# Kernel tuning notes

Measured on AMD Instinct MI355X. Metric: run time of the kernel, lower is better.

## Reference

```python
import jax, jax.numpy as jnp
import numpy as np

H, C, D, F = 8, 1024, 128, 512  # num_heads, num_chanels, out_dim, featurs_dim
B = 16


def setup_inputs() -> dict:
    key = jax.random.key(0)
    ks = jax.random.split(key, 9)
    s = 0.02
    return {
        "x": jax.random.normal(ks[0], (B, C, F), jnp.float32),
        "Wk": jax.random.normal(ks[1], (F, H * D), jnp.float32) * s,
        "bk": jax.random.normal(ks[2], (H * D,), jnp.float32) * s,
        "Wq": jax.random.normal(ks[3], (F, H * D), jnp.float32) * s,
        "bq": jax.random.normal(ks[4], (H * D,), jnp.float32) * s,
        "Wv": jax.random.normal(ks[5], (F, H * D), jnp.float32) * s,
        "bv": jax.random.normal(ks[6], (H * D,), jnp.float32) * s,
        "Ww0": jax.random.normal(ks[7], (H * D, D), jnp.float32) * s,
        "bw0": jax.random.normal(ks[8], (D,), jnp.float32) * s,
    }


def reference(x, Wk, bk, Wq, bq, Wv, bv, Ww0, bw0):
    # Linear projections on last dim: [B, C, H*D]
    # NOTE: the original reshapes [B, C, H*D] -> [B, H, C, D] WITHOUT a permute,
    # which mixes channel/head axes; we replicate that exactly.
    k = (x @ Wk + bk).reshape(-1, H, C, D)
    q = (x @ Wq + bq).reshape(-1, H, C, D)
    v = (x @ Wv + bv).reshape(-1, H, C, D)
    scores = jnp.einsum('bhcf,bhdf->bhcd', q, k) / jnp.sqrt(jnp.float32(D))
    att = jax.nn.softmax(scores, axis=-1) - jnp.eye(C, dtype=scores.dtype)
    vals = jnp.einsum('bhcd,bhdf->bhcf', att, v)          # [B, H, C, D]
    vals = vals.transpose(0, 2, 1, 3).reshape(vals.shape[0], C, H * D)
    return vals @ Ww0 + bw0                                # [B, C, D]
```

## Files before the change

kernel.cpp:

```cpp
#include <hip/hip_runtime.h>
#include <hip/hip_bf16.h>
#include <cstdint>
#include <cstddef>

using u16 = unsigned short;
typedef __attribute__((ext_vector_type(4))) float f32x4;
typedef __attribute__((ext_vector_type(16))) float f32x16;
typedef __attribute__((ext_vector_type(8))) unsigned short u16x8;
typedef __attribute__((ext_vector_type(4))) unsigned short u16x4;
typedef __attribute__((ext_vector_type(4))) unsigned int u32x4;
typedef __bf16 bfrag __attribute__((ext_vector_type(8)));

constexpr int Hn = 8, Cn = 1024, Dn = 128, Fn = 512, Bn = 16;
constexpr int M1 = Bn * Cn;

constexpr size_t OFF_XB  = 0;
constexpr size_t SZ_XB   = (size_t)M1 * Fn * 2;
constexpr size_t OFF_WT  = OFF_XB + SZ_XB;
constexpr size_t SZ_WT   = 3ull * 1024 * 512 * 2;
constexpr size_t OFF_W0T = OFF_WT + SZ_WT;
constexpr size_t SZ_W0T  = 128ull * 1024 * 2;
constexpr size_t OFF_Q   = OFF_W0T + SZ_W0T;
constexpr size_t SZ_P    = (size_t)Bn * Hn * Cn * Dn * 2;
constexpr size_t OFF_K   = OFF_Q + SZ_P;
constexpr size_t OFF_V   = OFF_K + SZ_P;
constexpr size_t OFF_ATT = OFF_V + SZ_P;

__device__ __forceinline__ float bf2f(u16 u) {
  unsigned int x = ((unsigned int)u) << 16;
  return __builtin_bit_cast(float, x);
}
__device__ __forceinline__ u16 f2bf(float f) {
  unsigned int u = __builtin_bit_cast(unsigned int, f);
  u += 0x7fffu + ((u >> 16) & 1u);
  return (u16)(u >> 16);
}
__device__ __forceinline__ f32x4 mfma16(bfrag a, bfrag b, f32x4 c) {
  return __builtin_amdgcn_mfma_f32_16x16x32_bf16(a, b, c, 0, 0, 0);
}
__device__ __forceinline__ f32x16 mfma32(bfrag a, bfrag b, f32x16 c) {
  return __builtin_amdgcn_mfma_f32_32x32x16_bf16(a, b, c, 0, 0, 0);
}
__device__ __forceinline__ void gload16(const void* g, void* lds) {
  __builtin_amdgcn_global_load_lds(
      (const __attribute__((address_space(1))) unsigned int*)g,
      (__attribute__((address_space(3))) unsigned int*)lds, 16, 0, 0);
}
__device__ __forceinline__ unsigned cvtpk(float lo, float hi) {
  unsigned r;
  asm("v_cvt_pk_bf16_f32 %0, %1, %2" : "=v"(r) : "v"(lo), "v"(hi));
  return r;
}

__global__ void cvt_bf16(const float* __restrict__ in, u16* __restrict__ out, int n) {
  int idx = (blockIdx.x * blockDim.x + threadIdx.x) * 4;
  if (idx < n) {
    float4 v = *(const float4*)(in + idx);
    u16x4 o;
    o.x = f2bf(v.x); o.y = f2bf(v.y); o.z = f2bf(v.z); o.w = f2bf(v.w);
    *(u16x4*)(out + idx) = o;
  }
}

__global__ void transpose_cvt(const float* __restrict__ in, u16* __restrict__ out,
                              int R, int Cc) {
  __shared__ float tile[32][33];
  int c0 = blockIdx.x * 32, r0 = blockIdx.y * 32;
  int tx = threadIdx.x, ty = threadIdx.y;
#pragma unroll
  for (int i = 0; i < 4; ++i)
    tile[ty + i * 8][tx] = in[(size_t)(r0 + ty + i * 8) * Cc + c0 + tx];
  __syncthreads();
#pragma unroll
  for (int i = 0; i < 4; ++i)
    out[(size_t)(c0 + ty + i * 8) * R + r0 + tx] = f2bf(tile[tx][ty + i * 8]);
}

__global__ void vtrans(const u16* __restrict__ in, u16* __restrict__ out) {
  __shared__ u16 tile[32][33];
  int d0 = blockIdx.x * 32, c0 = blockIdx.y * 32, bh = blockIdx.z;
  const u16* ip = in + (size_t)bh * (Cn * Dn);
  u16* op = out + (size_t)bh * (Dn * Cn);
  int tx = threadIdx.x, ty = threadIdx.y;
#pragma unroll
  for (int i = 0; i < 4; ++i)
    tile[ty + i * 8][tx] = ip[(size_t)(c0 + ty + i * 8) * Dn + d0 + tx];
  __syncthreads();
#pragma unroll
  for (int i = 0; i < 4; ++i)
    op[(size_t)(d0 + ty + i * 8) * Cn + c0 + tx] = tile[tx][ty + i * 8];
}

__global__ void qkv_gemm(const u16* __restrict__ xb, const u16* __restrict__ wt,
                         const float* __restrict__ bq, const float* __restrict__ bk,
                         const float* __restrict__ bv,
                         u16* __restrict__ qout, u16* __restrict__ kout,
                         u16* __restrict__ vout) {
  __shared__ u16 As[128 * 64];
  __shared__ u16 Bs[128 * 64];
  const int m0 = blockIdx.x * 128;
  const int n0 = blockIdx.y * 128;
  const int p  = blockIdx.z;
  const u16* wp = wt + (size_t)p * 1024 * 512;
  const float* bias = (p == 0) ? bq : (p == 1) ? bk : bv;
  u16* outp = (p == 0) ? qout : (p == 1) ? kout : vout;
  const float osc = (p == 0) ? 0.12751744116389548f : 1.0f;

  const int tid = threadIdx.x, l = tid & 63, w = tid >> 6;
  const int lr = l & 15, lg = l >> 4;
  const int wr = w >> 1, wc = w & 1;

  f32x4 acc[4][4] = {};

  for (int kt = 0; kt < Fn; kt += 64) {
#pragma unroll
    for (int i = 0; i < 4; ++i) {
      int chb = (i * 4 + w) * 64;
      int ch = chb + l;
      int row = ch >> 3, scc = (ch & 7) ^ (row & 7);
      gload16(xb + (size_t)(m0 + row) * Fn + kt + scc * 8, &As[chb * 8]);
    }
#pragma unroll
    for (int i = 0; i < 4; ++i) {
      int chb = (i * 4 + w) * 64;
      int ch = chb + l;
      int row = ch >> 3, scc = (ch & 7) ^ (row & 7);
      gload16(wp + (size_t)(n0 + row) * Fn + kt + scc * 8, &Bs[chb * 8]);
    }
    __syncthreads();
#pragma unroll
    for (int kk = 0; kk < 2; ++kk) {
      bfrag af[4], bf_[4];
#pragma unroll
      for (int fm = 0; fm < 4; ++fm) {
        int row = wr * 64 + fm * 16 + lr;
        int off = (kk * 4 + lg) ^ (row & 7);
        af[fm] = *(const bfrag*)&As[row * 64 + off * 8];
      }
#pragma unroll
      for (int fn = 0; fn < 4; ++fn) {
        int row = wc * 64 + fn * 16 + lr;
        int off = (kk * 4 + lg) ^ (row & 7);
        bf_[fn] = *(const bfrag*)&Bs[row * 64 + off * 8];
      }
#pragma unroll
      for (int fm = 0; fm < 4; ++fm)
#pragma unroll
        for (int fn = 0; fn < 4; ++fn)
          acc[fm][fn] = mfma16(af[fm], bf_[fn], acc[fm][fn]);
    }
    __syncthreads();
  }

#pragma unroll
  for (int fm = 0; fm < 4; ++fm) {
#pragma unroll
    for (int r = 0; r < 4; ++r) {
      int m = m0 + wr * 64 + fm * 16 + lg * 4 + r;
      int b = m >> 10, c = m & 1023;
      int gh = c >> 7;
#pragma unroll
      for (int fn = 0; fn < 4; ++fn) {
        int j = n0 + wc * 64 + fn * 16 + lr;
        float v = (acc[fm][fn][r] + bias[j]) * osc;
        int ii = ((c & 127) << 3) | (j >> 7);
        int d = j & 127;
        size_t idx = (((size_t)(b * 8 + gh) * 1024 + ii) << 7) | d;
        outp[idx] = f2bf(v);
      }
    }
  }
}

__global__ __launch_bounds__(256, 2)
void attn_kernel(const u16* __restrict__ qp_all, const u16* __restrict__ kp_all,
                 const u16* __restrict__ vt_all, u16* __restrict__ attout) {
  __shared__ u16 smem[2 * 16384];

  const int bid = blockIdx.x;
  const int wg = (bid & 7) * 128 + (bid >> 3);
  const int bh = wg >> 3;
  const int qt = wg & 7;

  const int tid = threadIdx.x, l = tid & 63, w = tid >> 6;
  const int q31 = l & 31, hi = l >> 5;

  const u16* qp  = qp_all + (size_t)bh * (Cn * Dn);
  const u16* kp  = kp_all + (size_t)bh * (Cn * Dn);
  const u16* vtp = vt_all + (size_t)bh * (Dn * Cn);
  const int qr0 = qt * 128 + w * 32;

  auto stage = [&](int t2, int b) {
    const u16* kb = kp + (size_t)t2 * 64 * 128;
    const u16* vb = vtp + (size_t)t2 * 64;
    u16* KsD = smem + b * 16384;
    u16* VsD = smem + b * 16384 + 8192;
#pragma unroll
    for (int c = 0; c < 4; ++c) {
      int ch = c * 256 + tid;
      int row = ch >> 4, scc = (ch & 15) ^ (row & 15);
      gload16(kb + row * 128 + scc * 8, KsD + (c * 256 + w * 64) * 8);
    }
#pragma unroll
    for (int c = 0; c < 4; ++c) {
      int ch = c * 256 + tid;
      int row = ch >> 3, scc = (ch & 7) ^ (row & 7);
      gload16(vb + (size_t)row * 1024 + scc * 8, VsD + (c * 256 + w * 64) * 8);
    }
  };

  bfrag aq[8];
#pragma unroll
  for (int kk = 0; kk < 8; ++kk)
    aq[kk] = *(const bfrag*)(qp + (size_t)(qr0 + q31) * Dn + kk * 16 + hi * 8);

  f32x16 ot[4] = {};
  float mst = -1e30f, lst = 0.f;

  stage(0, 0);
  __syncthreads();

  for (int t = 0; t < 16; ++t) {
    const int cur = t & 1;
    const u16* Ks = smem + cur * 16384;
    const u16* Vs = smem + cur * 16384 + 8192;
    if (t < 15) stage(t + 1, cur ^ 1);

    f32x16 st[2] = {};
    __builtin_amdgcn_s_setprio(1);
#pragma unroll
    for (int tt = 0; tt < 2; ++tt) {
#pragma unroll
      for (int kk = 0; kk < 8; ++kk) {
        int row = tt * 32 + q31;
        int off = (2 * kk + hi) ^ (row & 15);
        bfrag kf = *(const bfrag*)&Ks[row * 128 + off * 8];
        st[tt] = mfma32(kf, aq[kk], st[tt]);
      }
    }
    __builtin_amdgcn_s_setprio(0);

    float mx = st[0][0];
#pragma unroll
    for (int r = 1; r < 16; ++r) mx = fmaxf(mx, st[0][r]);
#pragma unroll
    for (int r = 0; r < 16; ++r) mx = fmaxf(mx, st[1][r]);
    mx = fmaxf(mx, __shfl_xor(mx, 32, 64));
    if (!__all(mx <= mst + 8.f)) {
      float mnew = fmaxf(mst, mx);
      float alpha = exp2f(mst - mnew);
      lst *= alpha;
#pragma unroll
      for (int dt = 0; dt < 4; ++dt)
#pragma unroll
        for (int r = 0; r < 16; ++r) ot[dt][r] *= alpha;
      mst = mnew;
    }
    float rs = 0.f;
#pragma unroll
    for (int tt = 0; tt < 2; ++tt)
#pragma unroll
      for (int r = 0; r < 16; ++r) {
        float pv = exp2f(st[tt][r] - mst);
        st[tt][r] = pv;
        rs += pv;
      }
    rs += __shfl_xor(rs, 32, 64);
    lst += rs;

    bfrag pb[4];
#pragma unroll
    for (int tt = 0; tt < 2; ++tt) {
      unsigned c[8];
#pragma unroll
      for (int m = 0; m < 8; ++m)
        c[m] = cvtpk(st[tt][2 * m], st[tt][2 * m + 1]);
#pragma unroll
      for (int kkt = 0; kkt < 2; ++kkt) {
        unsigned a0 = c[4 * kkt + 0], b0 = c[4 * kkt + 2];
        unsigned a1 = c[4 * kkt + 1], b1 = c[4 * kkt + 3];
        asm("v_permlane32_swap_b32 %0, %1" : "+v"(a0), "+v"(b0));
        asm("v_permlane32_swap_b32 %0, %1" : "+v"(a1), "+v"(b1));
        u32x4 bw; bw.x = a0; bw.y = a1; bw.z = b0; bw.w = b1;
        pb[tt * 2 + kkt] = __builtin_bit_cast(bfrag, bw);
      }
    }

    __builtin_amdgcn_s_setprio(1);
#pragma unroll
    for (int kk = 0; kk < 4; ++kk) {
#pragma unroll
      for (int dt = 0; dt < 4; ++dt) {
        int d = dt * 32 + q31;
        int off = (2 * kk + hi) ^ (d & 7);
        bfrag vf = *(const bfrag*)&Vs[d * 64 + off * 8];
        ot[dt] = mfma32(vf, pb[kk], ot[dt]);
      }
    }
    __builtin_amdgcn_s_setprio(0);
    __syncthreads();
  }

  const float linv = 1.f / lst;
  const int c1 = qr0 + q31;
  u16* my = smem + w * 4096;
#pragma unroll
  for (int dt = 0; dt < 4; ++dt)
#pragma unroll
    for (int rp = 0; rp < 8; ++rp) {
      int reg = 2 * rp;
      int d = dt * 32 + (reg & 3) + 8 * (reg >> 2) + 4 * hi;
      float v0 = bf2f(vtp[((size_t)d << 10) | c1]);
      float v1 = bf2f(vtp[((size_t)(d + 1) << 10) | c1]);
      unsigned pk = cvtpk(ot[dt][reg] * linv - v0, ot[dt][reg + 1] * linv - v1);
      *(unsigned*)&my[q31 * 128 + (((d >> 3) ^ (q31 & 7)) << 3) + (d & 7)] = pk;
    }
  const int b = bh >> 3, h = bh & 7;
#pragma unroll
  for (int it = 0; it < 8; ++it) {
    int rowq = it * 4 + (l >> 4);
    int ch = l & 15;
    u16x8 rd = *(const u16x8*)&my[rowq * 128 + ((ch ^ (rowq & 7))) * 8];
    int cg = qr0 + rowq;
    *(u16x8*)&attout[(((size_t)(b * 1024 + cg)) * 8 + h) * 128 + ch * 8] = rd;
  }
}

__global__ void out_gemm(const u16* __restrict__ A, const u16* __restrict__ Bt,
                         const float* __restrict__ bias, float* __restrict__ out) {
  __shared__ u16 As[64 * 64];
  __shared__ u16 Bs[128 * 64];
  const int m0 = blockIdx.x * 64;
  const int tid = threadIdx.x, l = tid & 63, w = tid >> 6;
  const int lr = l & 15, lg = l >> 4;
  const int wr = w >> 1, wc = w & 1;
  f32x4 acc[2][4] = {};

  for (int kt = 0; kt < 1024; kt += 64) {
#pragma unroll
    for (int i = 0; i < 2; ++i) {
      int chb = (i * 4 + w) * 64;
      int ch = chb + l;
      int row = ch >> 3, scc = (ch & 7) ^ (row & 7);
      gload16(A + (size_t)(m0 + row) * 1024 + kt + scc * 8, &As[chb * 8]);
    }
#pragma unroll
    for (int i = 0; i < 4; ++i) {
      int chb = (i * 4 + w) * 64;
      int ch = chb + l;
      int row = ch >> 3, scc = (ch & 7) ^ (row & 7);
      gload16(Bt + (size_t)row * 1024 + kt + scc * 8, &Bs[chb * 8]);
    }
    __syncthreads();
#pragma unroll
    for (int kk = 0; kk < 2; ++kk) {
      bfrag af[2], bf_[4];
#pragma unroll
      for (int fm = 0; fm < 2; ++fm) {
        int row = wr * 32 + fm * 16 + lr;
        int off = (kk * 4 + lg) ^ (row & 7);
        af[fm] = *(const bfrag*)&As[row * 64 + off * 8];
      }
#pragma unroll
      for (int fn = 0; fn < 4; ++fn) {
        int row = wc * 64 + fn * 16 + lr;
        int off = (kk * 4 + lg) ^ (row & 7);
        bf_[fn] = *(const bfrag*)&Bs[row * 64 + off * 8];
      }
#pragma unroll
      for (int fm = 0; fm < 2; ++fm)
#pragma unroll
        for (int fn = 0; fn < 4; ++fn)
          acc[fm][fn] = mfma16(af[fm], bf_[fn], acc[fm][fn]);
    }
    __syncthreads();
  }
#pragma unroll
  for (int fm = 0; fm < 2; ++fm)
#pragma unroll
    for (int r = 0; r < 4; ++r) {
      int m = m0 + wr * 32 + fm * 16 + lg * 4 + r;
#pragma unroll
      for (int fn = 0; fn < 4; ++fn) {
        int j = wc * 64 + fn * 16 + lr;
        out[(size_t)m * 128 + j] = acc[fm][fn][r] + bias[j];
      }
    }
}

extern "C" void kernel_launch(void* const* d_in, const int* in_sizes, int n_in,
                              void* d_out, int out_size, void* d_ws, size_t ws_size,
                              hipStream_t stream) {
  const float* x   = (const float*)d_in[0];
  const float* Wk  = (const float*)d_in[1];
  const float* bk_ = (const float*)d_in[2];
  const float* Wq  = (const float*)d_in[3];
  const float* bq_ = (const float*)d_in[4];
  const float* Wv  = (const float*)d_in[5];
  const float* bv_ = (const float*)d_in[6];
  const float* Ww0 = (const float*)d_in[7];
  const float* bw0 = (const float*)d_in[8];
  float* out = (float*)d_out;

  char* ws = (char*)d_ws;
  u16* xb   = (u16*)(ws + OFF_XB);
  u16* wt   = (u16*)(ws + OFF_WT);
  u16* w0t  = (u16*)(ws + OFF_W0T);
  u16* qpm  = (u16*)(ws + OFF_Q);
  u16* kpm  = (u16*)(ws + OFF_K);
  u16* vpm  = (u16*)(ws + OFF_V);
  u16* attb = (u16*)(ws + OFF_ATT);

  cvt_bf16<<<(M1 * Fn / 4 + 255) / 256, 256, 0, stream>>>(x, xb, M1 * Fn);
  dim3 tb(32, 8);
  transpose_cvt<<<dim3(32, 16), tb, 0, stream>>>(Wq, wt + 0 * 1024 * 512, 512, 1024);
  transpose_cvt<<<dim3(32, 16), tb, 0, stream>>>(Wk, wt + 1 * 1024 * 512, 512, 1024);
  transpose_cvt<<<dim3(32, 16), tb, 0, stream>>>(Wv, wt + 2 * 1024 * 512, 512, 1024);
  transpose_cvt<<<dim3(4, 32),  tb, 0, stream>>>(Ww0, w0t, 1024, 128);

  qkv_gemm<<<dim3(128, 8, 3), 256, 0, stream>>>(xb, wt, bq_, bk_, bv_, qpm, kpm, attb);

  vtrans<<<dim3(4, 32, 128), tb, 0, stream>>>(attb, vpm);

  attn_kernel<<<dim3(1024), 256, 0, stream>>>(qpm, kpm, vpm, attb);

  out_gemm<<<256, 256, 0, stream>>>(attb, w0t, bw0, out);
}
```

Measured before the change: 204.8 us.

## Merge QKV weight transposes, precompute attention LDS addresses, retile output GEMM

The three separate Q/K/V weight transpose launches become one launch over a z-dimension. The attention kernel now precomputes per-thread global and LDS byte offsets with XOR-based buffer toggling. Its max and sum reductions become tree and multi-accumulator forms to shorten dependency chains. The output GEMM switches to 32-row tiles with 512 blocks to raise parallelism, at the cost of reloading the B tile in more blocks.

```diff
diff --git a/kernel.cpp b/kernel.cpp
--- a/kernel.cpp
+++ b/kernel.cpp
@@ -74,6 +74,23 @@
 #pragma unroll
   for (int i = 0; i < 4; ++i)
     out[(size_t)(c0 + ty + i * 8) * R + r0 + tx] = f2bf(tile[tx][ty + i * 8]);
+}
+
+__global__ void transpose_cvt3(const float* __restrict__ W0, const float* __restrict__ W1,
+                               const float* __restrict__ W2, u16* __restrict__ out) {
+  __shared__ float tile[32][33];
+  const int z = blockIdx.z;
+  const float* in = (z == 0) ? W0 : (z == 1) ? W1 : W2;
+  u16* op = out + (size_t)z * 1024 * 512;
+  int c0 = blockIdx.x * 32, r0 = blockIdx.y * 32;
+  int tx = threadIdx.x, ty = threadIdx.y;
+#pragma unroll
+  for (int i = 0; i < 4; ++i)
+    tile[ty + i * 8][tx] = in[(size_t)(r0 + ty + i * 8) * 1024 + c0 + tx];
+  __syncthreads();
+#pragma unroll
+  for (int i = 0; i < 4; ++i)
+    op[(size_t)(c0 + ty + i * 8) * 512 + r0 + tx] = f2bf(tile[tx][ty + i * 8]);
 }
 
 __global__ void vtrans(const u16* __restrict__ in, u16* __restrict__ out) {
@@ -176,6 +193,7 @@
 void attn_kernel(const u16* __restrict__ qp_all, const u16* __restrict__ kp_all,
                  const u16* __restrict__ vt_all, u16* __restrict__ attout) {
   __shared__ u16 smem[2 * 16384];
+  char* smb = (char*)smem;
 
   const int bid = blockIdx.x;
   const int wg = (bid & 7) * 128 + (bid >> 3);
@@ -190,23 +208,28 @@
   const u16* vtp = vt_all + (size_t)bh * (Dn * Cn);
   const int qr0 = qt * 128 + w * 32;
 
-  auto stage = [&](int t2, int b) {
-    const u16* kb = kp + (size_t)t2 * 64 * 128;
-    const u16* vb = vtp + (size_t)t2 * 64;
-    u16* KsD = smem + b * 16384;
-    u16* VsD = smem + b * 16384 + 8192;
-#pragma unroll
-    for (int c = 0; c < 4; ++c) {
-      int ch = c * 256 + tid;
-      int row = ch >> 4, scc = (ch & 15) ^ (row & 15);
-      gload16(kb + row * 128 + scc * 8, KsD + (c * 256 + w * 64) * 8);
-    }
-#pragma unroll
-    for (int c = 0; c < 4; ++c) {
-      int ch = c * 256 + tid;
-      int row = ch >> 3, scc = (ch & 7) ^ (row & 7);
-      gload16(vb + (size_t)row * 1024 + scc * 8, VsD + (c * 256 + w * 64) * 8);
-    }
+  const unsigned LK = (unsigned)(q31 * 256) ^ (unsigned)((q31 & 15) * 16) ^ (unsigned)(hi * 16);
+  const unsigned LV = 16384u ^ (unsigned)(q31 * 128) ^ (unsigned)((q31 & 7) * 16) ^ (unsigned)(hi * 16);
+
+  const u16* ksrc[4]; const u16* vsrc[4];
+  unsigned kdst[4], vdst[4];
+#pragma unroll
+  for (int c = 0; c < 4; ++c) {
+    int ch = c * 256 + tid;
+    int krow = ch >> 4, kscc = (ch & 15) ^ (krow & 15);
+    ksrc[c] = kp + krow * 128 + kscc * 8;
+    int vrow = ch >> 3, vscc = (ch & 7) ^ (vrow & 7);
+    vsrc[c] = vtp + (size_t)vrow * 1024 + vscc * 8;
+    kdst[c] = (unsigned)((c * 256 + w * 64) * 16);
+    vdst[c] = 16384u + (unsigned)((c * 256 + w * 64) * 16);
+  }
+  auto stage = [&](int t2, unsigned bufb) {
+#pragma unroll
+    for (int c = 0; c < 4; ++c)
+      gload16(ksrc[c] + (size_t)t2 * 8192, smb + (bufb ^ kdst[c]));
+#pragma unroll
+    for (int c = 0; c < 4; ++c)
+      gload16(vsrc[c] + (size_t)t2 * 64, smb + (bufb ^ vdst[c]));
   };
 
   bfrag aq[8];
@@ -220,32 +243,34 @@
   stage(0, 0);
   __syncthreads();
 
+  unsigned bufb = 0;
   for (int t = 0; t < 16; ++t) {
-    const int cur = t & 1;
-    const u16* Ks = smem + cur * 16384;
-    const u16* Vs = smem + cur * 16384 + 8192;
-    if (t < 15) stage(t + 1, cur ^ 1);
-
-    f32x16 st[2] = {};
+    const unsigned nb = bufb ^ 32768u;
+    if (t < 15) stage(t + 1, nb);
+    const unsigned LKb = LK ^ bufb;
+    const unsigned LVb = LV ^ bufb;
+
+    f32x16 st0 = {}, st1 = {};
     __builtin_amdgcn_s_setprio(1);
 #pragma unroll
-    for (int tt = 0; tt < 2; ++tt) {
-#pragma unroll
-      for (int kk = 0; kk < 8; ++kk) {
-        int row = tt * 32 + q31;
-        int off = (2 * kk + hi) ^ (row & 15);
-        bfrag kf = *(const bfrag*)&Ks[row * 128 + off * 8];
-        st[tt] = mfma32(kf, aq[kk], st[tt]);
-      }
+    for (int kk = 0; kk < 8; ++kk) {
+      bfrag k0 = *(const bfrag*)(smb + (LKb ^ (unsigned)(kk * 32)));
+      st0 = mfma32(k0, aq[kk], st0);
+      bfrag k1 = *(const bfrag*)(smb + (LKb ^ (unsigned)(8192 + kk * 32)));
+      st1 = mfma32(k1, aq[kk], st1);
     }
     __builtin_amdgcn_s_setprio(0);
 
-    float mx = st[0][0];
-#pragma unroll
-    for (int r = 1; r < 16; ++r) mx = fmaxf(mx, st[0][r]);
-#pragma unroll
-    for (int r = 0; r < 16; ++r) mx = fmaxf(mx, st[1][r]);
-    mx = fmaxf(mx, __shfl_xor(mx, 32, 64));
+    float mxp[8];
+#pragma unroll
+    for (int i = 0; i < 8; ++i)
+      mxp[i] = fmaxf(fmaxf(st0[2 * i], st0[2 * i + 1]),
+                     fmaxf(st1[2 * i], st1[2 * i + 1]));
+#pragma unroll
+    for (int s2 = 4; s2 > 0; s2 >>= 1)
+#pragma unroll
+      for (int i = 0; i < s2; ++i) mxp[i] = fmaxf(mxp[i], mxp[i + s2]);
+    float mx = fmaxf(mxp[0], __shfl_xor(mxp[0], 32, 64));
     if (!__all(mx <= mst + 8.f)) {
       float mnew = fmaxf(mst, mx);
       float alpha = exp2f(mst - mnew);
@@ -256,33 +281,48 @@
         for (int r = 0; r < 16; ++r) ot[dt][r] *= alpha;
       mst = mnew;
     }
-    float rs = 0.f;
-#pragma unroll
-    for (int tt = 0; tt < 2; ++tt)
-#pragma unroll
-      for (int r = 0; r < 16; ++r) {
-        float pv = exp2f(st[tt][r] - mst);
-        st[tt][r] = pv;
-        rs += pv;
-      }
+    float rp[4] = {0.f, 0.f, 0.f, 0.f};
+#pragma unroll
+    for (int r = 0; r < 16; ++r) {
+      float p0 = exp2f(st0[r] - mst);
+      st0[r] = p0;
+      rp[r & 3] += p0;
+    }
+#pragma unroll
+    for (int r = 0; r < 16; ++r) {
+      float p1 = exp2f(st1[r] - mst);
+      st1[r] = p1;
+      rp[r & 3] += p1;
+    }
+    float rs = (rp[0] + rp[1]) + (rp[2] + rp[3]);
     rs += __shfl_xor(rs, 32, 64);
     lst += rs;
 
     bfrag pb[4];
-#pragma unroll
-    for (int tt = 0; tt < 2; ++tt) {
-      unsigned c[8];
-#pragma unroll
-      for (int m = 0; m < 8; ++m)
-        c[m] = cvtpk(st[tt][2 * m], st[tt][2 * m + 1]);
+    {
+      unsigned c0_[8], c1_[8];
+#pragma unroll
+      for (int m = 0; m < 8; ++m) {
+        c0_[m] = cvtpk(st0[2 * m], st0[2 * m + 1]);
+        c1_[m] = cvtpk(st1[2 * m], st1[2 * m + 1]);
+      }
 #pragma unroll
       for (int kkt = 0; kkt < 2; ++kkt) {
-        unsigned a0 = c[4 * kkt + 0], b0 = c[4 * kkt + 2];
-        unsigned a1 = c[4 * kkt + 1], b1 = c[4 * kkt + 3];
+        unsigned a0 = c0_[4 * kkt + 0], b0 = c0_[4 * kkt + 2];
+        unsigned a1 = c0_[4 * kkt + 1], b1 = c0_[4 * kkt + 3];
         asm("v_permlane32_swap_b32 %0, %1" : "+v"(a0), "+v"(b0));
         asm("v_permlane32_swap_b32 %0, %1" : "+v"(a1), "+v"(b1));
         u32x4 bw; bw.x = a0; bw.y = a1; bw.z = b0; bw.w = b1;
-        pb[tt * 2 + kkt] = __builtin_bit_cast(bfrag, bw);
+        pb[kkt] = __builtin_bit_cast(bfrag, bw);
+      }
+#pragma unroll
+      for (int kkt = 0; kkt < 2; ++kkt) {
+        unsigned a0 = c1_[4 * kkt + 0], b0 = c1_[4 * kkt + 2];
+        unsigned a1 = c1_[4 * kkt + 1], b1 = c1_[4 * kkt + 3];
+        asm("v_permlane32_swap_b32 %0, %1" : "+v"(a0), "+v"(b0));
+        asm("v_permlane32_swap_b32 %0, %1" : "+v"(a1), "+v"(b1));
+        u32x4 bw; bw.x = a0; bw.y = a1; bw.z = b0; bw.w = b1;
+        pb[2 + kkt] = __builtin_bit_cast(bfrag, bw);
       }
     }
 
@@ -291,14 +331,13 @@
     for (int kk = 0; kk < 4; ++kk) {
 #pragma unroll
       for (int dt = 0; dt < 4; ++dt) {
-        int d = dt * 32 + q31;
-        int off = (2 * kk + hi) ^ (d & 7);
-        bfrag vf = *(const bfrag*)&Vs[d * 64 + off * 8];
+        bfrag vf = *(const bfrag*)(smb + (LVb ^ (unsigned)(dt * 4096 + kk * 32)));
         ot[dt] = mfma32(vf, pb[kk], ot[dt]);
       }
     }
     __builtin_amdgcn_s_setprio(0);
     __syncthreads();
+    bufb = nb;
   }
 
   const float linv = 1.f / lst;
@@ -307,8 +346,8 @@
 #pragma unroll
   for (int dt = 0; dt < 4; ++dt)
 #pragma unroll
-    for (int rp = 0; rp < 8; ++rp) {
-      int reg = 2 * rp;
+    for (int rp2 = 0; rp2 < 8; ++rp2) {
+      int reg = 2 * rp2;
       int d = dt * 32 + (reg & 3) + 8 * (reg >> 2) + 4 * hi;
       float v0 = bf2f(vtp[((size_t)d << 10) | c1]);
       float v1 = bf2f(vtp[((size_t)(d + 1) << 10) | c1]);
@@ -328,21 +367,18 @@
 
 __global__ void out_gemm(const u16* __restrict__ A, const u16* __restrict__ Bt,
                          const float* __restrict__ bias, float* __restrict__ out) {
-  __shared__ u16 As[64 * 64];
+  __shared__ u16 As[32 * 64];
   __shared__ u16 Bs[128 * 64];
-  const int m0 = blockIdx.x * 64;
+  const int m0 = blockIdx.x * 32;
   const int tid = threadIdx.x, l = tid & 63, w = tid >> 6;
   const int lr = l & 15, lg = l >> 4;
-  const int wr = w >> 1, wc = w & 1;
-  f32x4 acc[2][4] = {};
+  f32x4 acc[2][2] = {};
 
   for (int kt = 0; kt < 1024; kt += 64) {
-#pragma unroll
-    for (int i = 0; i < 2; ++i) {
-      int chb = (i * 4 + w) * 64;
-      int ch = chb + l;
+    {
+      int ch = w * 64 + l;
       int row = ch >> 3, scc = (ch & 7) ^ (row & 7);
-      gload16(A + (size_t)(m0 + row) * 1024 + kt + scc * 8, &As[chb * 8]);
+      gload16(A + (size_t)(m0 + row) * 1024 + kt + scc * 8, &As[(w * 64) * 8]);
     }
 #pragma unroll
     for (int i = 0; i < 4; ++i) {
@@ -354,23 +390,23 @@
     __syncthreads();
 #pragma unroll
     for (int kk = 0; kk < 2; ++kk) {
-      bfrag af[2], bf_[4];
+      bfrag af[2], bf_[2];
 #pragma unroll
       for (int fm = 0; fm < 2; ++fm) {
-        int row = wr * 32 + fm * 16 + lr;
+        int row = fm * 16 + lr;
         int off = (kk * 4 + lg) ^ (row & 7);
         af[fm] = *(const bfrag*)&As[row * 64 + off * 8];
       }
 #pragma unroll
-      for (int fn = 0; fn < 4; ++fn) {
-        int row = wc * 64 + fn * 16 + lr;
+      for (int fn = 0; fn < 2; ++fn) {
+        int row = w * 32 + fn * 16 + lr;
         int off = (kk * 4 + lg) ^ (row & 7);
         bf_[fn] = *(const bfrag*)&Bs[row * 64 + off * 8];
       }
 #pragma unroll
       for (int fm = 0; fm < 2; ++fm)
 #pragma unroll
-        for (int fn = 0; fn < 4; ++fn)
+        for (int fn = 0; fn < 2; ++fn)
           acc[fm][fn] = mfma16(af[fm], bf_[fn], acc[fm][fn]);
     }
     __syncthreads();
@@ -379,10 +415,10 @@
   for (int fm = 0; fm < 2; ++fm)
 #pragma unroll
     for (int r = 0; r < 4; ++r) {
-      int m = m0 + wr * 32 + fm * 16 + lg * 4 + r;
-#pragma unroll
-      for (int fn = 0; fn < 4; ++fn) {
-        int j = wc * 64 + fn * 16 + lr;
+      int m = m0 + fm * 16 + lg * 4 + r;
+#pragma unroll
+      for (int fn = 0; fn < 2; ++fn) {
+        int j = w * 32 + fn * 16 + lr;
         out[(size_t)m * 128 + j] = acc[fm][fn][r] + bias[j];
       }
     }
@@ -413,10 +449,8 @@
 
   cvt_bf16<<<(M1 * Fn / 4 + 255) / 256, 256, 0, stream>>>(x, xb, M1 * Fn);
   dim3 tb(32, 8);
-  transpose_cvt<<<dim3(32, 16), tb, 0, stream>>>(Wq, wt + 0 * 1024 * 512, 512, 1024);
-  transpose_cvt<<<dim3(32, 16), tb, 0, stream>>>(Wk, wt + 1 * 1024 * 512, 512, 1024);
-  transpose_cvt<<<dim3(32, 16), tb, 0, stream>>>(Wv, wt + 2 * 1024 * 512, 512, 1024);
-  transpose_cvt<<<dim3(4, 32),  tb, 0, stream>>>(Ww0, w0t, 1024, 128);
+  transpose_cvt3<<<dim3(32, 16, 3), tb, 0, stream>>>(Wq, Wk, Wv, wt);
+  transpose_cvt<<<dim3(4, 32), tb, 0, stream>>>(Ww0, w0t, 1024, 128);
 
   qkv_gemm<<<dim3(128, 8, 3), 256, 0, stream>>>(xb, wt, bq_, bk_, bv_, qpm, kpm, attb);
 
@@ -424,5 +458,5 @@
 
   attn_kernel<<<dim3(1024), 256, 0, stream>>>(qpm, kpm, vpm, attb);
 
-  out_gemm<<<256, 256, 0, stream>>>(attb, w0t, bw0, out);
-}
+  out_gemm<<<512, 256, 0, stream>>>(attb, w0t, bw0, out);
+}
```

New measurement: 198.5 us. 1.03x faster.
